# Performance work log

Hardware: AMD Instinct MI355X
Metric: run time of the kernel (lower is better)

## Reference

```python
import jax, jax.numpy as jnp
import numpy as np

EPS = 1e-8  # torch.nn.CosineSimilarity eps


def setup_inputs() -> dict:
    key = jax.random.key(0)
    k1, k2, k3 = jax.random.split(key, 3)
    C, S, D = 1024, 16, 512
    x = jax.random.normal(k1, (C, S, D), dtype=jnp.float32)
    w = jax.random.normal(k2, (1,), dtype=jnp.float32)
    b = jax.random.normal(k3, (1,), dtype=jnp.float32)
    return {"x": x, "w": w, "b": b}


def reference(x, w, b):
    # stable_ge2e: leave-one-out positive centroids, full negative centroids.
    C, S, D = x.shape
    wp = jax.nn.softplus(w)  # (1,)

    sum_c = x.sum(axis=1)                      # (C, D)
    mean_c = sum_c / S                         # negative centroids (C, D)
    loo = (sum_c[:, None, :] - x) / (S - 1.0)  # leave-one-out centroids (C, S, D)

    nx = jnp.linalg.norm(x, axis=-1)           # (C, S)
    nmean = jnp.linalg.norm(mean_c, axis=-1)   # (C,)
    nloo = jnp.linalg.norm(loo, axis=-1)       # (C, S)

    # cosine similarities (clamped denominator, as in torch CosineSimilarity)
    sim_neg = jnp.einsum('jid,kd->jik', x, mean_c) / jnp.maximum(
        nx[:, :, None] * nmean[None, None, :], EPS)          # (C, S, C)
    sim_pos = jnp.einsum('jid,jid->ji', x, loo) / jnp.maximum(nx * nloo, EPS)  # (C, S)

    # on the diagonal k == j use the leave-one-out positive centroid
    eye = jnp.eye(C, dtype=bool)
    sim = jnp.where(eye[:, None, :], sim_pos[:, :, None], sim_neg)  # (C, S, C)

    logits = wp * sim + b
    logS = jax.nn.log_softmax(logits, axis=-1)
    Sji_j = jnp.einsum('jij->ji', logS)                        # (C, S) diagonal
    Sji_k = jax.scipy.special.logsumexp(logS, axis=-1)         # (C, S) (== 0 post-softmax)
    loss = -(Sji_j - Sji_k).reshape(-1)
    return loss.mean()
```

## Files before the change

kernel.cpp:

```cpp
#include <hip/hip_runtime.h>
#include <math.h>

#define CC 1024
#define SS 16
#define DD 512
#define RR (CC*SS)
#define EPSV 1e-8f
#define LDB 520
#define LDX 516
#define CHUNK 32
#define NCHUNK 16

typedef __attribute__((ext_vector_type(8))) short short8;
typedef __attribute__((ext_vector_type(4))) float f32x4;
typedef unsigned short ushort_t;

__device__ __forceinline__ unsigned short f2bf(float f) {
  unsigned u = __float_as_uint(f);
  u += 0x7fffu + ((u >> 16) & 1u);
  return (unsigned short)(u >> 16);
}

__device__ __forceinline__ void async16(void* l, const void* g) {
  __builtin_amdgcn_global_load_lds(
      (const __attribute__((address_space(1))) void*)g,
      (__attribute__((address_space(3))) void*)l, 16, 0, 0);
}

__device__ __forceinline__ float softplusf(float v) {
  return (v > 20.f) ? v : log1pf(expf(v));
}

#define SBAR()   __builtin_amdgcn_s_barrier()
#define SCHED0() __builtin_amdgcn_sched_barrier(0)

__global__ __launch_bounds__(256) void k_pre(
    const float* __restrict__ x, ushort_t* __restrict__ mn,
    float* __restrict__ nx, float* __restrict__ simpos,
    ushort_t* __restrict__ xn) {
  __shared__ float xs[SS * LDX];
  __shared__ float sums[DD];
  __shared__ float colpart[1024];
  __shared__ float red[4];
  __shared__ float rinv[SS];
  const int j = blockIdx.x, tid = threadIdx.x;
  const int wid = tid >> 6, lane = tid & 63;
  const float4* xj = (const float4*)(x + (size_t)j * SS * DD);

  const int half = tid >> 7;
  const int col4 = tid & 127;
  float4 cs = {0.f, 0.f, 0.f, 0.f};
#pragma unroll
  for (int i = 0; i < 8; ++i) {
    const int row = half * 8 + i;
    const float4 v = xj[row * 128 + col4];
    cs.x += v.x; cs.y += v.y; cs.z += v.z; cs.w += v.w;
    *(float4*)(xs + row * LDX + col4 * 4) = v;
  }
  ((float4*)colpart)[tid] = cs;
  __syncthreads();

  float4 s4 = {0.f, 0.f, 0.f, 0.f};
  float m2 = 0.f;
  if (tid < 128) {
    const float4 lo = ((const float4*)colpart)[tid];
    const float4 hi = ((const float4*)colpart)[tid + 128];
    s4.x = lo.x + hi.x; s4.y = lo.y + hi.y;
    s4.z = lo.z + hi.z; s4.w = lo.w + hi.w;
    ((float4*)sums)[tid] = s4;
    const float mx = s4.x * (1.f / SS), my = s4.y * (1.f / SS);
    const float mz = s4.z * (1.f / SS), mw = s4.w * (1.f / SS);
    m2 = mx * mx + my * my + mz * mz + mw * mw;
  }
#pragma unroll
  for (int off = 32; off > 0; off >>= 1) m2 += __shfl_xor(m2, off, 64);
  if (lane == 0) red[wid] = m2;
  __syncthreads();
  const float snm = sqrtf(red[0] + red[1] + red[2] + red[3]);
  const float inm = (1.0f / SS) / snm;
  if (tid < 128) {
    uint2 o;
    o.x = (unsigned)f2bf(s4.x * inm) | ((unsigned)f2bf(s4.y * inm) << 16);
    o.y = (unsigned)f2bf(s4.z * inm) | ((unsigned)f2bf(s4.w * inm) << 16);
    ((uint2*)(mn + (size_t)j * DD))[tid] = o;
  }

  {
    const int g = tid >> 4, l16 = tid & 15;
    float nx2 = 0.f, dxs = 0.f, t2 = 0.f;
#pragma unroll
    for (int t = 0; t < 8; ++t) {
      const int c = l16 + t * 16;
      const float4 xv = *(const float4*)(xs + g * LDX + c * 4);
      const float4 sc = ((const float4*)sums)[c];
      nx2 = fmaf(xv.x, xv.x, fmaf(xv.y, xv.y,
            fmaf(xv.z, xv.z, fmaf(xv.w, xv.w, nx2))));
      dxs = fmaf(xv.x, sc.x, fmaf(xv.y, sc.y,
            fmaf(xv.z, sc.z, fmaf(xv.w, sc.w, dxs))));
      const float ax = sc.x - xv.x, ay = sc.y - xv.y;
      const float az = sc.z - xv.z, aw = sc.w - xv.w;
      t2 = fmaf(ax, ax, fmaf(ay, ay, fmaf(az, az, fmaf(aw, aw, t2))));
    }
#pragma unroll
    for (int off = 1; off < 16; off <<= 1) {
      nx2 += __shfl_xor(nx2, off, 64);
      dxs += __shfl_xor(dxs, off, 64);
      t2  += __shfl_xor(t2,  off, 64);
    }
    if (l16 == 0) {
      const float nxv = sqrtf(nx2);
      const float tn  = sqrtf(t2);
      const float num = (dxs - nx2) * (1.0f / (SS - 1));
      const float den = fmaxf(nxv * tn * (1.0f / (SS - 1)), EPSV);
      nx[j * SS + g] = nxv;
      rinv[g] = 1.0f / nxv;
      simpos[j * SS + g] = num / den;
    }
  }
  __syncthreads();

  if (xn) {
    uint4* dst = (uint4*)xn + (size_t)j * 1024;
#pragma unroll
    for (int t = 0; t < 4; ++t) {
      const int idxu = tid + t * 256;
      const int kc = idxu >> 6, quad = (idxu >> 4) & 3, cL = idxu & 15;
      const float* s = xs + cL * LDX + kc * 32 + quad * 8;
      const float4 a = *(const float4*)s;
      const float4 b2 = *(const float4*)(s + 4);
      const float ri = rinv[cL];
      uint4 o;
      o.x = (unsigned)f2bf(a.x * ri) | ((unsigned)f2bf(a.y * ri) << 16);
      o.y = (unsigned)f2bf(a.z * ri) | ((unsigned)f2bf(a.w * ri) << 16);
      o.z = (unsigned)f2bf(b2.x * ri) | ((unsigned)f2bf(b2.y * ri) << 16);
      o.w = (unsigned)f2bf(b2.z * ri) | ((unsigned)f2bf(b2.w * ri) << 16);
      dst[idxu] = o;
    }
  }
}

template <bool USE_XN>
__global__ __launch_bounds__(128, 2) void k_gemm(
    const float* __restrict__ x, const ushort_t* __restrict__ xn,
    const ushort_t* __restrict__ mn, const float* __restrict__ nx,
    const float* __restrict__ simpos, const float* __restrict__ wptr,
    const float* __restrict__ bptr, float* __restrict__ ps) {
  __shared__ ushort_t bs[2][CHUNK * LDB];
  const int tid = threadIdx.x;
  const int wid = tid >> 6, lane = tid & 63;
  const int cL = lane & 15, quad = lane >> 4;
  const int bid = (int)blockIdx.x;
  const int rb = bid & 255, cb = bid >> 8;
  const int r0 = rb * 64, cbase = cb * 512;
  const float wp = softplusf(wptr[0]), bv = bptr[0];
  const int row0w = r0 + wid * 32;

  {
    const ushort_t* gsrc = mn + (size_t)cbase * DD;
#pragma unroll
    for (int t = 0; t < 16; ++t) {
      const int rr = wid + t * 2;
      async16(&bs[0][rr * LDB + lane * 8], gsrc + (size_t)rr * DD + lane * 8);
    }
  }

  short8 af[2][16];
  int jw[2];
  float sp[2][4], sacc[2][4];
#pragma unroll
  for (int rt = 0; rt < 2; ++rt) {
    jw[rt] = (row0w + rt * 16) >> 4;
    if (USE_XN) {
      const short8* xw = (const short8*)xn + (size_t)jw[rt] * 1024;
#pragma unroll
      for (int kc = 0; kc < 16; ++kc) af[rt][kc] = xw[kc * 64 + lane];
    } else {
      const int row = row0w + rt * 16 + cL;
      const float* xr = x + (size_t)row * DD;
      const float invn = 1.0f / nx[row];
#pragma unroll
      for (int kc = 0; kc < 16; ++kc) {
        const int k0 = kc * 32 + quad * 8;
        float4 p = *(const float4*)(xr + k0);
        float4 q = *(const float4*)(xr + k0 + 4);
        short8 v;
        v[0] = f2bf(p.x * invn); v[1] = f2bf(p.y * invn);
        v[2] = f2bf(p.z * invn); v[3] = f2bf(p.w * invn);
        v[4] = f2bf(q.x * invn); v[5] = f2bf(q.y * invn);
        v[6] = f2bf(q.z * invn); v[7] = f2bf(q.w * invn);
        af[rt][kc] = v;
      }
    }
#pragma unroll
    for (int r = 0; r < 4; ++r) {
      sp[rt][r] = simpos[row0w + rt * 16 + quad * 4 + r];
      sacc[rt][r] = 0.f;
    }
  }

#pragma unroll
  for (int cc = 0; cc < NCHUNK; ++cc) {
    if (cc < NCHUNK - 1) {
      const ushort_t* gsrc = mn + (size_t)(cbase + (cc + 1) * CHUNK) * DD;
      ushort_t* dst = bs[(cc + 1) & 1];
#pragma unroll
      for (int t = 0; t < 16; ++t) {
        const int rr = wid + t * 2;
        async16(&dst[rr * LDB + lane * 8], gsrc + (size_t)rr * DD + lane * 8);
      }
      SCHED0();
      asm volatile("s_waitcnt vmcnt(16)" ::: "memory");
    } else {
      asm volatile("s_waitcnt vmcnt(0)" ::: "memory");
    }
    SCHED0();
    SBAR();
    SCHED0();

    const ushort_t* B = bs[cc & 1];
    f32x4 acc[2][2];
#pragma unroll
    for (int rt = 0; rt < 2; ++rt)
#pragma unroll
      for (int f = 0; f < 2; ++f) acc[rt][f] = (f32x4){0.f, 0.f, 0.f, 0.f};
    __builtin_amdgcn_s_setprio(1);
#pragma unroll
    for (int kc = 0; kc < 16; ++kc) {
      short8 bfr[2];
#pragma unroll
      for (int f = 0; f < 2; ++f)
        bfr[f] = *(const short8*)&B[(f * 16 + cL) * LDB + kc * 32 + quad * 8];
#pragma unroll
      for (int rt = 0; rt < 2; ++rt)
#pragma unroll
        for (int f = 0; f < 2; ++f)
          acc[rt][f] = __builtin_amdgcn_mfma_f32_16x16x32_bf16(
              af[rt][kc], bfr[f], acc[rt][f], 0, 0, 0);
    }
    __builtin_amdgcn_s_setprio(0);
    if (cc < NCHUNK - 1) {
      SCHED0();
      SBAR();
      SCHED0();
    }
    const int c0 = cbase + cc * CHUNK;
#pragma unroll
    for (int rt = 0; rt < 2; ++rt)
#pragma unroll
      for (int f = 0; f < 2; ++f) {
        const int cg = c0 + f * 16 + cL;
        const bool diag = (cg == jw[rt]);
#pragma unroll
        for (int r = 0; r < 4; ++r) {
          const float sim = diag ? sp[rt][r] : acc[rt][f][r];
          sacc[rt][r] += __expf(fmaf(wp, sim, bv));
        }
      }
  }

#pragma unroll
  for (int rt = 0; rt < 2; ++rt)
#pragma unroll
    for (int r = 0; r < 4; ++r) {
      float v = sacc[rt][r];
#pragma unroll
      for (int off = 1; off < 16; off <<= 1) v += __shfl_xor(v, off, 64);
      if (cL == 0)
        ps[(size_t)(row0w + rt * 16 + quad * 4 + r) * 2 + cb] = v;
    }
}

__global__ __launch_bounds__(256) void k_combine(
    const float* __restrict__ ps, const float* __restrict__ simpos,
    const float* __restrict__ wptr, const float* __restrict__ bptr,
    float* __restrict__ p2) {
  __shared__ float red[4];
  const int tid = threadIdx.x;
  const int row = blockIdx.x * 256 + tid;
  const float wp = softplusf(wptr[0]), bv = bptr[0];
  const float2 v2 = ((const float2*)ps)[row];
  float v = logf(v2.x + v2.y) - fmaf(wp, simpos[row], bv);
#pragma unroll
  for (int off = 32; off > 0; off >>= 1) v += __shfl_xor(v, off, 64);
  if ((tid & 63) == 0) red[tid >> 6] = v;
  __syncthreads();
  if (tid == 0) p2[blockIdx.x] = red[0] + red[1] + red[2] + red[3];
}

__global__ __launch_bounds__(64) void k_fin(const float* __restrict__ p2,
                                            float* __restrict__ out) {
  const int tid = threadIdx.x;
  float v = p2[tid];
#pragma unroll
  for (int off = 32; off > 0; off >>= 1) v += __shfl_xor(v, off, 64);
  if (tid == 0) out[0] = v * (1.0f / RR);
}

extern "C" void kernel_launch(void* const* d_in, const int* in_sizes, int n_in,
                              void* d_out, int out_size, void* d_ws, size_t ws_size,
                              hipStream_t stream) {
  const float* x = (const float*)d_in[0];
  const float* w = (const float*)d_in[1];
  const float* b = (const float*)d_in[2];
  float* out = (float*)d_out;

  const size_t xn_bytes = (size_t)RR * DD * 2;
  const size_t rest = (size_t)CC * DD * 2 + (size_t)RR * 4 * 2 +
                      (size_t)RR * 2 * 4 + 64 * 4;
  const bool use_xn = ws_size >= xn_bytes + rest + 256;

  char* base = (char*)d_ws;
  ushort_t* xn = use_xn ? (ushort_t*)base : nullptr;
  char* p = base + (use_xn ? xn_bytes : 0);
  ushort_t* mn = (ushort_t*)p;  p += (size_t)CC * DD * 2;
  float* nx     = (float*)p;    p += (size_t)RR * 4;
  float* simpos = (float*)p;    p += (size_t)RR * 4;
  float* ps     = (float*)p;    p += (size_t)RR * 2 * 4;
  float* p2     = (float*)p;

  k_pre<<<CC, 256, 0, stream>>>(x, mn, nx, simpos, xn);
  if (use_xn)
    k_gemm<true><<<512, 128, 0, stream>>>(x, xn, mn, nx, simpos, w, b, ps);
  else
    k_gemm<false><<<512, 128, 0, stream>>>(x, xn, mn, nx, simpos, w, b, ps);
  k_combine<<<RR / 256, 256, 0, stream>>>(ps, simpos, w, b, p2);
  k_fin<<<1, 64, 0, stream>>>(p2, out);
}
```

Measured before the change: 109.9 us.

## Split GEMM column range into four blocks and halve B chunk width

The similarity GEMM now splits the 1024 centroid columns into four 256-column ranges instead of two, doubling the grid to 1024 blocks. The LDS B chunk shrinks from 32 to 16 columns, so each wave does two MFMAs per k-step instead of four. The exp/accumulate epilogue moves before the trailing barrier and the s_setprio hints are dropped. The aim is more blocks for better occupancy and latency hiding on MI355X, at the cost of reloading the A fragments twice as often, smaller MFMA batches per barrier, and a larger partial-sum buffer that the combine kernel must read.

```diff
diff --git a/kernel.cpp b/kernel.cpp
--- a/kernel.cpp
+++ b/kernel.cpp
@@ -8,7 +8,7 @@
 #define EPSV 1e-8f
 #define LDB 520
 #define LDX 516
-#define CHUNK 32
+#define CHUNK 16
 #define NCHUNK 16
 
 typedef __attribute__((ext_vector_type(8))) short short8;
@@ -151,14 +151,14 @@
   const int cL = lane & 15, quad = lane >> 4;
   const int bid = (int)blockIdx.x;
   const int rb = bid & 255, cb = bid >> 8;
-  const int r0 = rb * 64, cbase = cb * 512;
+  const int r0 = rb * 64, cbase = cb * 256;
   const float wp = softplusf(wptr[0]), bv = bptr[0];
   const int row0w = r0 + wid * 32;
 
   {
     const ushort_t* gsrc = mn + (size_t)cbase * DD;
 #pragma unroll
-    for (int t = 0; t < 16; ++t) {
+    for (int t = 0; t < 8; ++t) {
       const int rr = wid + t * 2;
       async16(&bs[0][rr * LDB + lane * 8], gsrc + (size_t)rr * DD + lane * 8);
     }
@@ -204,12 +204,12 @@
       const ushort_t* gsrc = mn + (size_t)(cbase + (cc + 1) * CHUNK) * DD;
       ushort_t* dst = bs[(cc + 1) & 1];
 #pragma unroll
-      for (int t = 0; t < 16; ++t) {
+      for (int t = 0; t < 8; ++t) {
         const int rr = wid + t * 2;
         async16(&dst[rr * LDB + lane * 8], gsrc + (size_t)rr * DD + lane * 8);
       }
       SCHED0();
-      asm volatile("s_waitcnt vmcnt(16)" ::: "memory");
+      asm volatile("s_waitcnt vmcnt(8)" ::: "memory");
     } else {
       asm volatile("s_waitcnt vmcnt(0)" ::: "memory");
     }
@@ -218,44 +218,34 @@
     SCHED0();
 
     const ushort_t* B = bs[cc & 1];
-    f32x4 acc[2][2];
-#pragma unroll
-    for (int rt = 0; rt < 2; ++rt)
-#pragma unroll
-      for (int f = 0; f < 2; ++f) acc[rt][f] = (f32x4){0.f, 0.f, 0.f, 0.f};
-    __builtin_amdgcn_s_setprio(1);
+    f32x4 acc[2];
+    acc[0] = (f32x4){0.f, 0.f, 0.f, 0.f};
+    acc[1] = (f32x4){0.f, 0.f, 0.f, 0.f};
 #pragma unroll
     for (int kc = 0; kc < 16; ++kc) {
-      short8 bfr[2];
-#pragma unroll
-      for (int f = 0; f < 2; ++f)
-        bfr[f] = *(const short8*)&B[(f * 16 + cL) * LDB + kc * 32 + quad * 8];
-#pragma unroll
-      for (int rt = 0; rt < 2; ++rt)
-#pragma unroll
-        for (int f = 0; f < 2; ++f)
-          acc[rt][f] = __builtin_amdgcn_mfma_f32_16x16x32_bf16(
-              af[rt][kc], bfr[f], acc[rt][f], 0, 0, 0);
-    }
-    __builtin_amdgcn_s_setprio(0);
+      const short8 bfr =
+          *(const short8*)&B[cL * LDB + kc * 32 + quad * 8];
+      acc[0] = __builtin_amdgcn_mfma_f32_16x16x32_bf16(af[0][kc], bfr,
+                                                       acc[0], 0, 0, 0);
+      acc[1] = __builtin_amdgcn_mfma_f32_16x16x32_bf16(af[1][kc], bfr,
+                                                       acc[1], 0, 0, 0);
+    }
+    const int c0 = cbase + cc * CHUNK;
+#pragma unroll
+    for (int rt = 0; rt < 2; ++rt) {
+      const int cg = c0 + cL;
+      const bool diag = (cg == jw[rt]);
+#pragma unroll
+      for (int r = 0; r < 4; ++r) {
+        const float sim = diag ? sp[rt][r] : acc[rt][r];
+        sacc[rt][r] += __expf(fmaf(wp, sim, bv));
+      }
+    }
     if (cc < NCHUNK - 1) {
       SCHED0();
       SBAR();
       SCHED0();
     }
-    const int c0 = cbase + cc * CHUNK;
-#pragma unroll
-    for (int rt = 0; rt < 2; ++rt)
-#pragma unroll
-      for (int f = 0; f < 2; ++f) {
-        const int cg = c0 + f * 16 + cL;
-        const bool diag = (cg == jw[rt]);
-#pragma unroll
-        for (int r = 0; r < 4; ++r) {
-          const float sim = diag ? sp[rt][r] : acc[rt][f][r];
-          sacc[rt][r] += __expf(fmaf(wp, sim, bv));
-        }
-      }
   }
 
 #pragma unroll
@@ -266,7 +256,7 @@
 #pragma unroll
       for (int off = 1; off < 16; off <<= 1) v += __shfl_xor(v, off, 64);
       if (cL == 0)
-        ps[(size_t)(row0w + rt * 16 + quad * 4 + r) * 2 + cb] = v;
+        ps[(size_t)(row0w + rt * 16 + quad * 4 + r) * 4 + cb] = v;
     }
 }
 
@@ -278,8 +268,9 @@
   const int tid = threadIdx.x;
   const int row = blockIdx.x * 256 + tid;
   const float wp = softplusf(wptr[0]), bv = bptr[0];
-  const float2 v2 = ((const float2*)ps)[row];
-  float v = logf(v2.x + v2.y) - fmaf(wp, simpos[row], bv);
+  const f32x4 v4 = ((const f32x4*)ps)[row];
+  const float s = (v4[0] + v4[1]) + (v4[2] + v4[3]);
+  float v = logf(s) - fmaf(wp, simpos[row], bv);
 #pragma unroll
   for (int off = 32; off > 0; off >>= 1) v += __shfl_xor(v, off, 64);
   if ((tid & 63) == 0) red[tid >> 6] = v;
@@ -306,7 +297,7 @@
 
   const size_t xn_bytes = (size_t)RR * DD * 2;
   const size_t rest = (size_t)CC * DD * 2 + (size_t)RR * 4 * 2 +
-                      (size_t)RR * 2 * 4 + 64 * 4;
+                      (size_t)RR * 4 * 4 + 64 * 4;
   const bool use_xn = ws_size >= xn_bytes + rest + 256;
 
   char* base = (char*)d_ws;
@@ -315,14 +306,14 @@
   ushort_t* mn = (ushort_t*)p;  p += (size_t)CC * DD * 2;
   float* nx     = (float*)p;    p += (size_t)RR * 4;
   float* simpos = (float*)p;    p += (size_t)RR * 4;
-  float* ps     = (float*)p;    p += (size_t)RR * 2 * 4;
+  float* ps     = (float*)p;    p += (size_t)RR * 4 * 4;
   float* p2     = (float*)p;
 
   k_pre<<<CC, 256, 0, stream>>>(x, mn, nx, simpos, xn);
   if (use_xn)
-    k_gemm<true><<<512, 128, 0, stream>>>(x, xn, mn, nx, simpos, w, b, ps);
+    k_gemm<true><<<1024, 128, 0, stream>>>(x, xn, mn, nx, simpos, w, b, ps);
   else
-    k_gemm<false><<<512, 128, 0, stream>>>(x, xn, mn, nx, simpos, w, b, ps);
+    k_gemm<false><<<1024, 128, 0, stream>>>(x, xn, mn, nx, simpos, w, b, ps);
   k_combine<<<RR / 256, 256, 0, stream>>>(ps, simpos, w, b, p2);
   k_fin<<<1, 64, 0, stream>>>(p2, out);
 }
```

Measured after the change: 108.7 us. Within noise of the previous version (-1.1%).
